# Performance work log

Hardware: AMD Instinct MI355X
Metric: run time of the kernel (lower is better)

The kernel has to match this reference:

```python
import jax, jax.numpy as jnp
import numpy as np

EPS = 1e-5

def _layernorm(x, g, b):
    mu = jnp.mean(x, axis=-1, keepdims=True)
    var = jnp.mean(jnp.square(x - mu), axis=-1, keepdims=True)
    return (x - mu) * jax.lax.rsqrt(var + EPS) * g + b

def _mlp(x, w1, b1, w2, b2):
    h = jax.nn.gelu(jnp.einsum('bnd,dh->bnh', x, w1) + b1, approximate=False)
    return jnp.einsum('bnh,hd->bnd', h, w2) + b2

def setup_inputs() -> dict:
    key = jax.random.key(0)
    B, N, D, H = 2, 8192, 1024, 4096
    ks = jax.random.split(key, 12)
    s1 = 1.0 / np.sqrt(D)
    s2 = 1.0 / np.sqrt(H)
    return {
        'x': jax.random.normal(ks[0], (B, N, D), dtype=jnp.float32),
        'mask': jax.random.randint(ks[1], (B, N), 0, 2) > 0,
        'g_rgb': jnp.ones((D,), jnp.float32),
        'b_rgb': jnp.zeros((D,), jnp.float32),
        'w1_rgb': jax.random.normal(ks[2], (D, H), dtype=jnp.float32) * s1,
        'b1_rgb': jnp.zeros((H,), jnp.float32),
        'w2_rgb': jax.random.normal(ks[3], (H, D), dtype=jnp.float32) * s2,
        'b2_rgb': jnp.zeros((D,), jnp.float32),
        'g_expr': jnp.ones((D,), jnp.float32),
        'b_expr': jnp.zeros((D,), jnp.float32),
        'w1_expr': jax.random.normal(ks[4], (D, H), dtype=jnp.float32) * s1,
        'b1_expr': jnp.zeros((H,), jnp.float32),
        'w2_expr': jax.random.normal(ks[5], (H, D), dtype=jnp.float32) * s2,
        'b2_expr': jnp.zeros((D,), jnp.float32),
    }

def reference(x, mask, g_rgb, b_rgb, w1_rgb, b1_rgb, w2_rgb, b2_rgb,
              g_expr, b_expr, w1_expr, b1_expr, w2_expr, b2_expr):
    # Per-token routing: rgb expert where mask, expr expert where ~mask.
    # LayerNorm+MLP are pointwise per token, so dense compute + select is
    # mathematically identical to the torch gather->compute->scatter.
    z_rgb = _mlp(_layernorm(x, g_rgb, b_rgb), w1_rgb, b1_rgb, w2_rgb, b2_rgb)
    z_expr = _mlp(_layernorm(x, g_expr, b_expr), w1_expr, b1_expr, w2_expr, b2_expr)
    z = jnp.where(mask[..., None], z_rgb, z_expr)
    return z.astype(jnp.float16)  # torch scatters into a float16 buffer
```

## Files before the change

### kernel.cpp

```cpp
#include <hip/hip_runtime.h>
#include <hip/hip_bf16.h>
#include <hip/hip_fp16.h>

#define D_ 1024
#define H_ 4096
#define NTOK 16384
#define MPAD 16512

typedef __attribute__((ext_vector_type(8))) short bf16x8;
typedef __attribute__((ext_vector_type(4))) float f32x4;

static __device__ __forceinline__ unsigned short f2bf(float f) {
  union { float f; unsigned u; } x; x.f = f;
  unsigned u = x.u + 0x7fffu + ((x.u >> 16) & 1u);
  return (unsigned short)(u >> 16);
}

static __device__ __forceinline__ void gld16(const void* g, void* l) {
  __builtin_amdgcn_global_load_lds(
      (const __attribute__((address_space(1))) unsigned int*)g,
      (__attribute__((address_space(3))) unsigned int*)l, 16, 0, 0);
}

static __device__ __forceinline__ float gelu_fast(float x) {
  const float z = x * (1.5957691216f + 0.0713548163f * x * x);
  return x * __builtin_amdgcn_rcpf(1.0f + __expf(-z));
}

__global__ __launch_bounds__(256) void transpose4_kernel(
    const float* __restrict__ w1r, const float* __restrict__ w1e,
    const float* __restrict__ w2r, const float* __restrict__ w2e,
    unsigned short* __restrict__ o1r, unsigned short* __restrict__ o1e,
    unsigned short* __restrict__ o2r, unsigned short* __restrict__ o2e) {
  __shared__ float tile[32][33];
  const int t = blockIdx.x;
  const float* src; unsigned short* dst; int R, C, tl;
  if (t < 4096)       { src = w1r; dst = o1r; R = D_; C = H_; tl = t; }
  else if (t < 8192)  { src = w1e; dst = o1e; R = D_; C = H_; tl = t - 4096; }
  else if (t < 12288) { src = w2r; dst = o2r; R = H_; C = D_; tl = t - 8192; }
  else                { src = w2e; dst = o2e; R = H_; C = D_; tl = t - 12288; }
  const int tc = C >> 5;
  const int r0 = (tl / tc) * 32, c0 = (tl % tc) * 32;
  const int tx = threadIdx.x & 31, ty = threadIdx.x >> 5;
#pragma unroll
  for (int i = 0; i < 32; i += 8)
    tile[ty + i][tx] = src[(size_t)(r0 + ty + i) * C + c0 + tx];
  __syncthreads();
#pragma unroll
  for (int i = 0; i < 32; i += 8)
    dst[(size_t)(c0 + ty + i) * R + r0 + tx] = f2bf(tile[tx][ty + i]);
}

__global__ __launch_bounds__(256) void compact_kernel(
    const int* __restrict__ mask, int* __restrict__ perm, int* __restrict__ counts) {
  const int NT = 256, CH = NTOK / NT;
  __shared__ int sm[NTOK];
  __shared__ int wsum[4];
  const int t = threadIdx.x;
  const int ln = t & 63, wv = t >> 6;
  for (int i = t; i < NTOK; i += NT) sm[i] = mask[i];
  for (int i = t; i < MPAD; i += NT) perm[i] = -1;
  __syncthreads();
  const int base = t * CH;
  int cnt = 0;
  for (int i = 0; i < CH; ++i) cnt += (sm[base + i] != 0);
  int sc = cnt;
#pragma unroll
  for (int o = 1; o < 64; o <<= 1) {
    int u = __shfl_up(sc, o, 64);
    if (ln >= o) sc += u;
  }
  if (ln == 63) wsum[wv] = sc;
  __syncthreads();
  int woff = 0;
#pragma unroll
  for (int j = 0; j < 4; ++j) woff += (j < wv) ? wsum[j] : 0;
  const int total1 = wsum[0] + wsum[1] + wsum[2] + wsum[3];
  if (t == 0) { counts[0] = total1; counts[1] = NTOK - total1; }
  const int excl = woff + sc - cnt;
  const int expr_base = ((total1 + 127) >> 7) << 7;
  int p1 = excl;
  int p0 = expr_base + (base - excl);
  for (int i = 0; i < CH; ++i) {
    const int idx = base + i;
    if (sm[idx] != 0) perm[p1++] = idx; else perm[p0++] = idx;
  }
}

__global__ __launch_bounds__(256) void ln_kernel(
    const float* __restrict__ x, const int* __restrict__ mask,
    const int* __restrict__ perm,
    const float* __restrict__ g_rgb, const float* __restrict__ b_rgb,
    const float* __restrict__ g_expr, const float* __restrict__ b_expr,
    unsigned short* __restrict__ xln) {
  const int i = blockIdx.x;
  const int t = perm[i];
  if (t < 0) return;
  const int tid = threadIdx.x;
  const float4 v = ((const float4*)(x + (size_t)t * D_))[tid];
  float s = v.x + v.y + v.z + v.w;
  float ss = v.x * v.x + v.y * v.y + v.z * v.z + v.w * v.w;
#pragma unroll
  for (int o = 32; o > 0; o >>= 1) {
    s += __shfl_xor(s, o, 64);
    ss += __shfl_xor(ss, o, 64);
  }
  __shared__ float red[8];
  const int wv = tid >> 6, ln = tid & 63;
  if (ln == 0) { red[wv] = s; red[4 + wv] = ss; }
  __syncthreads();
  s = red[0] + red[1] + red[2] + red[3];
  ss = red[4] + red[5] + red[6] + red[7];
  const float mu = s * (1.0f / D_);
  const float var = ss * (1.0f / D_) - mu * mu;
  const float rs = rsqrtf(var + 1e-5f);
  const bool rgb = mask[t] != 0;
  const float4 gv = ((const float4*)(rgb ? g_rgb : g_expr))[tid];
  const float4 bv = ((const float4*)(rgb ? b_rgb : b_expr))[tid];
  const unsigned short o0 = f2bf((v.x - mu) * rs * gv.x + bv.x);
  const unsigned short o1 = f2bf((v.y - mu) * rs * gv.y + bv.y);
  const unsigned short o2 = f2bf((v.z - mu) * rs * gv.z + bv.z);
  const unsigned short o3 = f2bf((v.w - mu) * rs * gv.w + bv.w);
  uint2 pk;
  pk.x = (unsigned)o0 | ((unsigned)o1 << 16);
  pk.y = (unsigned)o2 | ((unsigned)o3 << 16);
  *((uint2*)(xln + (size_t)i * D_ + tid * 4)) = pk;
}

template <int EP, int K, int N>
__global__ __launch_bounds__(256) void gemm_kernel(
    const unsigned short* __restrict__ A,
    const unsigned short* __restrict__ Wt_rgb,
    const unsigned short* __restrict__ Wt_expr,
    const float* __restrict__ bias_rgb,
    const float* __restrict__ bias_expr,
    const int* __restrict__ counts,
    const int* __restrict__ perm,
    void* __restrict__ OutP) {
  constexpr int BM = 128, BN = 128, BK = 64;
  constexpr int MT = MPAD / BM;
  constexpr int NT = N / BN;
  const int tid = threadIdx.x;
  const int id = blockIdx.x;
  const int xcd = id & 7;
  const int slot = id >> 3;
  const int p = xcd * ((MT * NT) / 8) + slot;
  const int m0 = (p / NT) * BM;
  const int n0 = (p % NT) * BN;
  const int cnt_rgb = counts[0];
  const unsigned short* Wt = (m0 < cnt_rgb) ? Wt_rgb : Wt_expr;
  const float* bias = (m0 < cnt_rgb) ? bias_rgb : bias_expr;

  __shared__ unsigned short As[BM * BK];
  __shared__ unsigned short Bs[BN * BK];

  f32x4 acc[4][4] = {};

  const int lane = tid & 63, wave = tid >> 6;
  const int wm = (wave & 1) * 64, wn = (wave >> 1) * 64;
  const int quad = lane >> 4, l16 = lane & 15;

  const char* Abase = (const char*)A;
  const char* Wbase = (const char*)Wt;
  const char* AsB = (const char*)As;
  const char* BsB = (const char*)Bs;

  int ag[4], bg[4], sl[4];
#pragma unroll
  for (int it = 0; it < 4; ++it) {
    const int s = it * 256 + tid;
    const int row = s >> 3;
    const int ks = ((s ^ row) & 7) * 8;
    ag[it] = ((m0 + row) * K + ks) * 2;
    bg[it] = ((n0 + row) * K + ks) * 2;
    sl[it] = s * 16;
  }
  int aoff[2][4], boff[2][4];
#pragma unroll
  for (int hh = 0; hh < 2; ++hh) {
    const int cb = hh * 4 + quad;
#pragma unroll
    for (int mi = 0; mi < 4; ++mi) {
      const int row = wm + mi * 16 + l16;
      aoff[hh][mi] = (row * BK + (((cb ^ row) & 7) << 3)) * 2;
    }
#pragma unroll
    for (int ni = 0; ni < 4; ++ni) {
      const int row = wn + ni * 16 + l16;
      boff[hh][ni] = (row * BK + (((cb ^ row) & 7) << 3)) * 2;
    }
  }

  for (int k0 = 0; k0 < K; k0 += BK) {
#pragma unroll
    for (int it = 0; it < 4; ++it) {
      gld16(Abase + ag[it], (void*)(AsB + sl[it]));
      gld16(Wbase + bg[it], (void*)(BsB + sl[it]));
      ag[it] += BK * 2;
      bg[it] += BK * 2;
    }
    __syncthreads();
#pragma unroll
    for (int hh = 0; hh < 2; ++hh) {
      bf16x8 a[4], b[4];
#pragma unroll
      for (int mi = 0; mi < 4; ++mi) a[mi] = *(const bf16x8*)(AsB + aoff[hh][mi]);
#pragma unroll
      for (int ni = 0; ni < 4; ++ni) b[ni] = *(const bf16x8*)(BsB + boff[hh][ni]);
#pragma unroll
      for (int mi = 0; mi < 4; ++mi)
#pragma unroll
        for (int ni = 0; ni < 4; ++ni)
          acc[mi][ni] = __builtin_amdgcn_mfma_f32_16x16x32_bf16(a[mi], b[ni], acc[mi][ni], 0, 0, 0);
    }
    __syncthreads();
  }

  float bv[4];
#pragma unroll
  for (int ni = 0; ni < 4; ++ni) bv[ni] = bias[n0 + wn + ni * 16 + l16];

#pragma unroll
  for (int mi = 0; mi < 4; ++mi) {
#pragma unroll
    for (int r = 0; r < 4; ++r) {
      const int row = m0 + wm + mi * 16 + quad * 4 + r;
      if (EP == 0) {
        unsigned short* orow = (unsigned short*)OutP + (size_t)row * N + n0 + wn + l16;
#pragma unroll
        for (int ni = 0; ni < 4; ++ni) {
          orow[ni * 16] = f2bf(gelu_fast(acc[mi][ni][r] + bv[ni]));
        }
      } else {
        const int p2 = perm[row];
        if (p2 < 0) continue;
        float* orow = (float*)OutP + (size_t)p2 * N + n0 + wn + l16;
#pragma unroll
        for (int ni = 0; ni < 4; ++ni) {
          float v = acc[mi][ni][r] + bv[ni];
          orow[ni * 16] = __half2float(__float2half_rn(v));
        }
      }
    }
  }
}

extern "C" void kernel_launch(void* const* d_in, const int* in_sizes, int n_in,
                              void* d_out, int out_size, void* d_ws, size_t ws_size,
                              hipStream_t stream) {
  const float* x       = (const float*)d_in[0];
  const int*   mask    = (const int*)d_in[1];
  const float* g_rgb   = (const float*)d_in[2];
  const float* b_rgb   = (const float*)d_in[3];
  const float* w1_rgb  = (const float*)d_in[4];
  const float* b1_rgb  = (const float*)d_in[5];
  const float* w2_rgb  = (const float*)d_in[6];
  const float* b2_rgb  = (const float*)d_in[7];
  const float* g_expr  = (const float*)d_in[8];
  const float* b_expr  = (const float*)d_in[9];
  const float* w1_expr = (const float*)d_in[10];
  const float* b1_expr = (const float*)d_in[11];
  const float* w2_expr = (const float*)d_in[12];
  const float* b2_expr = (const float*)d_in[13];

  char* w = (char*)d_ws;
  int* counts               = (int*)(w + 0);
  int* perm                 = (int*)(w + 256);
  unsigned short* w1t_rgb   = (unsigned short*)(w + 66560);
  unsigned short* w1t_expr  = (unsigned short*)(w + 8455168);
  unsigned short* w2t_rgb   = (unsigned short*)(w + 16843776);
  unsigned short* w2t_expr  = (unsigned short*)(w + 25232384);
  unsigned short* xln       = (unsigned short*)(w + 33620992);
  unsigned short* h         = (unsigned short*)(w + 67437568);

  compact_kernel<<<1, 256, 0, stream>>>(mask, perm, counts);

  transpose4_kernel<<<16384, 256, 0, stream>>>(
      w1_rgb, w1_expr, w2_rgb, w2_expr, w1t_rgb, w1t_expr, w2t_rgb, w2t_expr);

  ln_kernel<<<MPAD, 256, 0, stream>>>(x, mask, perm, g_rgb, b_rgb, g_expr, b_expr, xln);

  gemm_kernel<0, D_, H_><<<dim3((H_ / 128) * (MPAD / 128)), 256, 0, stream>>>(
      xln, w1t_rgb, w1t_expr, b1_rgb, b1_expr, counts, perm, h);

  gemm_kernel<1, H_, D_><<<dim3((D_ / 128) * (MPAD / 128)), 256, 0, stream>>>(
      h, w2t_rgb, w2t_expr, b2_rgb, b2_expr, counts, perm, d_out);
}
```

Before: 592.0 us.

## Add 256x256-tile 8-wave pipelined GEMM for first MLP layer

Replaces the first GEMM (LN output × W1 with GELU epilogue) with a new kernel using 256x256 output tiles, 512 threads, double-buffered LDS filled by direct global-to-LDS loads, and interleaved barrier-scheduled MFMA phases with raised priority. Expert segments are now padded to 256 rows so each tile uses a single expert weight, which grows MPAD and shifts the workspace offsets. The larger tile raises arithmetic intensity and cuts redundant global traffic. In exchange it adds a little padding compute and heavy register and LDS use: 128 KB of shared memory per block and 128 accumulator floats per thread.

```diff
diff --git a/kernel.cpp b/kernel.cpp
--- a/kernel.cpp
+++ b/kernel.cpp
@@ -5,7 +5,7 @@
 #define D_ 1024
 #define H_ 4096
 #define NTOK 16384
-#define MPAD 16512
+#define MPAD 16640
 
 typedef __attribute__((ext_vector_type(8))) short bf16x8;
 typedef __attribute__((ext_vector_type(4))) float f32x4;
@@ -78,7 +78,7 @@
   const int total1 = wsum[0] + wsum[1] + wsum[2] + wsum[3];
   if (t == 0) { counts[0] = total1; counts[1] = NTOK - total1; }
   const int excl = woff + sc - cnt;
-  const int expr_base = ((total1 + 127) >> 7) << 7;
+  const int expr_base = ((total1 + 255) >> 8) << 8;
   int p1 = excl;
   int p0 = expr_base + (base - excl);
   for (int i = 0; i < CH; ++i) {
@@ -125,6 +125,183 @@
   pk.x = (unsigned)o0 | ((unsigned)o1 << 16);
   pk.y = (unsigned)o2 | ((unsigned)o3 << 16);
   *((uint2*)(xln + (size_t)i * D_ + tid * 4)) = pk;
+}
+
+template <int K, int N>
+__global__ __launch_bounds__(512, 2) void gemm8_kernel(
+    const unsigned short* __restrict__ A,
+    const unsigned short* __restrict__ Wt_rgb,
+    const unsigned short* __restrict__ Wt_expr,
+    const float* __restrict__ bias_rgb,
+    const float* __restrict__ bias_expr,
+    const int* __restrict__ counts,
+    unsigned short* __restrict__ Out) {
+  constexpr int MT = MPAD / 256;
+  constexpr int NT = N / 256;
+  constexpr int ntk = K / 64;
+  constexpr int KH2 = 128 * K * 2;
+
+  const int tid = threadIdx.x;
+  const int id = blockIdx.x;
+  const int xcd = id & 7;
+  const int slot = id >> 3;
+  const int p = xcd * ((MT * NT) / 8) + slot;
+  const int m0 = (p / NT) * 256;
+  const int n0 = (p % NT) * 256;
+  const int cnt_rgb = counts[0];
+  const unsigned short* Wt = (m0 < cnt_rgb) ? Wt_rgb : Wt_expr;
+  const float* bias = (m0 < cnt_rgb) ? bias_rgb : bias_expr;
+
+  __shared__ unsigned short As[2][256 * 64];
+  __shared__ unsigned short Bs[2][256 * 64];
+
+  const int lane = tid & 63, wave = tid >> 6;
+  const int wr = wave >> 2, wc = wave & 3;
+  const int quad = lane >> 4, l16 = lane & 15;
+
+  f32x4 acc[8][4] = {};
+
+  const char* Abase = (const char*)A;
+  const char* Wbase = (const char*)Wt;
+
+  int agK0, agK1, bgK0, bgK1, sl0, sl1;
+  {
+    const int s0 = tid, s1 = 512 + tid;
+    const int r0 = s0 >> 3, r1 = s1 >> 3;
+    const int ks0 = ((s0 ^ r0) & 7) * 8, ks1 = ((s1 ^ r1) & 7) * 8;
+    agK0 = ((m0 + r0) * K + ks0) * 2;  agK1 = ((m0 + r1) * K + ks1) * 2;
+    bgK0 = ((n0 + r0) * K + ks0) * 2;  bgK1 = ((n0 + r1) * K + ks1) * 2;
+    sl0 = s0 * 16;  sl1 = s1 * 16;
+  }
+
+  int aoffL[2][2][4];
+  int boffL[2][4];
+#pragma unroll
+  for (int kk = 0; kk < 2; ++kk) {
+    const int cb = kk * 4 + quad;
+#pragma unroll
+    for (int mh = 0; mh < 2; ++mh)
+#pragma unroll
+      for (int mi = 0; mi < 4; ++mi) {
+        const int row = wr * 128 + mh * 64 + mi * 16 + l16;
+        aoffL[kk][mh][mi] = (row * 64 + ((cb ^ row) & 7) * 8) * 2;
+      }
+#pragma unroll
+    for (int ni = 0; ni < 4; ++ni) {
+      const int row = wc * 64 + ni * 16 + l16;
+      boffL[kk][ni] = (row * 64 + ((cb ^ row) & 7) * 8) * 2;
+    }
+  }
+
+  bf16x8 a0, a1, a2, a3;
+  bf16x8 bb[4];
+
+#define STAGE_A(T1, HA, Q) do { \
+    gld16(Abase + agK0 + (HA) * KH2 + (T1) * 128, (char*)As + (Q) * 32768 + (HA) * 16384 + sl0); \
+    gld16(Abase + agK1 + (HA) * KH2 + (T1) * 128, (char*)As + (Q) * 32768 + (HA) * 16384 + sl1); \
+  } while (0)
+#define STAGE_B(T2, HB, Q) do { \
+    gld16(Wbase + bgK0 + (HB) * KH2 + (T2) * 128, (char*)Bs + (Q) * 32768 + (HB) * 16384 + sl0); \
+    gld16(Wbase + bgK1 + (HB) * KH2 + (T2) * 128, (char*)Bs + (Q) * 32768 + (HB) * 16384 + sl1); \
+  } while (0)
+#define RD_A(P_, KK, MH) do { \
+    const char* _ab = (const char*)As + (P_) * 32768; \
+    a0 = *(const bf16x8*)(_ab + aoffL[KK][MH][0]); \
+    a1 = *(const bf16x8*)(_ab + aoffL[KK][MH][1]); \
+    a2 = *(const bf16x8*)(_ab + aoffL[KK][MH][2]); \
+    a3 = *(const bf16x8*)(_ab + aoffL[KK][MH][3]); \
+  } while (0)
+#define RD_B(P_, KK) do { \
+    const char* _bp = (const char*)Bs + (P_) * 32768; \
+    bb[0] = *(const bf16x8*)(_bp + boffL[KK][0]); \
+    bb[1] = *(const bf16x8*)(_bp + boffL[KK][1]); \
+    bb[2] = *(const bf16x8*)(_bp + boffL[KK][2]); \
+    bb[3] = *(const bf16x8*)(_bp + boffL[KK][3]); \
+  } while (0)
+#define MFMA16(MO) do { \
+    acc[(MO)+0][0] = __builtin_amdgcn_mfma_f32_16x16x32_bf16(a0, bb[0], acc[(MO)+0][0], 0, 0, 0); \
+    acc[(MO)+0][1] = __builtin_amdgcn_mfma_f32_16x16x32_bf16(a0, bb[1], acc[(MO)+0][1], 0, 0, 0); \
+    acc[(MO)+0][2] = __builtin_amdgcn_mfma_f32_16x16x32_bf16(a0, bb[2], acc[(MO)+0][2], 0, 0, 0); \
+    acc[(MO)+0][3] = __builtin_amdgcn_mfma_f32_16x16x32_bf16(a0, bb[3], acc[(MO)+0][3], 0, 0, 0); \
+    acc[(MO)+1][0] = __builtin_amdgcn_mfma_f32_16x16x32_bf16(a1, bb[0], acc[(MO)+1][0], 0, 0, 0); \
+    acc[(MO)+1][1] = __builtin_amdgcn_mfma_f32_16x16x32_bf16(a1, bb[1], acc[(MO)+1][1], 0, 0, 0); \
+    acc[(MO)+1][2] = __builtin_amdgcn_mfma_f32_16x16x32_bf16(a1, bb[2], acc[(MO)+1][2], 0, 0, 0); \
+    acc[(MO)+1][3] = __builtin_amdgcn_mfma_f32_16x16x32_bf16(a1, bb[3], acc[(MO)+1][3], 0, 0, 0); \
+    acc[(MO)+2][0] = __builtin_amdgcn_mfma_f32_16x16x32_bf16(a2, bb[0], acc[(MO)+2][0], 0, 0, 0); \
+    acc[(MO)+2][1] = __builtin_amdgcn_mfma_f32_16x16x32_bf16(a2, bb[1], acc[(MO)+2][1], 0, 0, 0); \
+    acc[(MO)+2][2] = __builtin_amdgcn_mfma_f32_16x16x32_bf16(a2, bb[2], acc[(MO)+2][2], 0, 0, 0); \
+    acc[(MO)+2][3] = __builtin_amdgcn_mfma_f32_16x16x32_bf16(a2, bb[3], acc[(MO)+2][3], 0, 0, 0); \
+    acc[(MO)+3][0] = __builtin_amdgcn_mfma_f32_16x16x32_bf16(a3, bb[0], acc[(MO)+3][0], 0, 0, 0); \
+    acc[(MO)+3][1] = __builtin_amdgcn_mfma_f32_16x16x32_bf16(a3, bb[1], acc[(MO)+3][1], 0, 0, 0); \
+    acc[(MO)+3][2] = __builtin_amdgcn_mfma_f32_16x16x32_bf16(a3, bb[2], acc[(MO)+3][2], 0, 0, 0); \
+    acc[(MO)+3][3] = __builtin_amdgcn_mfma_f32_16x16x32_bf16(a3, bb[3], acc[(MO)+3][3], 0, 0, 0); \
+  } while (0)
+
+#define KTILE(T_, P_, SA_, SB_, VMC_) do { \
+     \
+    RD_B(P_, 0); RD_A(P_, 0, 0); \
+    if (SA_) STAGE_A((T_) + 1, 0, (P_) ^ 1); \
+    __builtin_amdgcn_s_barrier(); \
+    __builtin_amdgcn_s_setprio(1); MFMA16(0); __builtin_amdgcn_s_setprio(0); \
+    __builtin_amdgcn_s_barrier(); \
+     \
+    RD_A(P_, 0, 1); \
+    if (SA_) STAGE_A((T_) + 1, 1, (P_) ^ 1); \
+    __builtin_amdgcn_s_barrier(); \
+    __builtin_amdgcn_s_setprio(1); MFMA16(4); __builtin_amdgcn_s_setprio(0); \
+    __builtin_amdgcn_s_barrier(); \
+     \
+    RD_B(P_, 1); RD_A(P_, 1, 0); \
+    __builtin_amdgcn_s_barrier(); \
+    __builtin_amdgcn_s_setprio(1); MFMA16(0); __builtin_amdgcn_s_setprio(0); \
+    __builtin_amdgcn_s_barrier(); \
+     \
+    RD_A(P_, 1, 1); \
+    if (SB_) { STAGE_B((T_) + 2, 0, P_); STAGE_B((T_) + 2, 1, P_); } \
+    __builtin_amdgcn_s_barrier(); \
+    __builtin_amdgcn_s_setprio(1); MFMA16(4); __builtin_amdgcn_s_setprio(0); \
+    if ((VMC_) == 4) { asm volatile("s_waitcnt vmcnt(4)" ::: "memory"); } \
+    else if ((VMC_) == 0) { asm volatile("s_waitcnt vmcnt(0)" ::: "memory"); } \
+    __builtin_amdgcn_sched_barrier(0); \
+    __builtin_amdgcn_s_barrier(); \
+  } while (0)
+
+  STAGE_A(0, 0, 0); STAGE_A(0, 1, 0);
+  STAGE_B(0, 0, 0); STAGE_B(0, 1, 0);
+  STAGE_B(1, 0, 1); STAGE_B(1, 1, 1);
+  asm volatile("s_waitcnt vmcnt(4)" ::: "memory");
+  __builtin_amdgcn_sched_barrier(0);
+  __builtin_amdgcn_s_barrier();
+
+  for (int tt = 0; tt < ntk / 2 - 1; ++tt) {
+    const int t0 = tt * 2;
+    KTILE(t0, 0, 1, 1, 4);
+    KTILE(t0 + 1, 1, 1, 1, 4);
+  }
+  KTILE(ntk - 2, 0, 1, 0, 0);
+  KTILE(ntk - 1, 1, 0, 0, -1);
+
+#undef KTILE
+#undef MFMA16
+#undef RD_B
+#undef RD_A
+#undef STAGE_B
+#undef STAGE_A
+
+  float bv[4];
+#pragma unroll
+  for (int ni = 0; ni < 4; ++ni) bv[ni] = bias[n0 + wc * 64 + ni * 16 + l16];
+#pragma unroll
+  for (int mi = 0; mi < 8; ++mi) {
+#pragma unroll
+    for (int r = 0; r < 4; ++r) {
+      const int row = m0 + wr * 128 + mi * 16 + quad * 4 + r;
+      unsigned short* orow = Out + (size_t)row * N + n0 + wc * 64 + l16;
+#pragma unroll
+      for (int ni = 0; ni < 4; ++ni)
+        orow[ni * 16] = f2bf(gelu_fast(acc[mi][ni][r] + bv[ni]));
+    }
+  }
 }
 
 template <int EP, int K, int N>
@@ -266,12 +443,12 @@
   char* w = (char*)d_ws;
   int* counts               = (int*)(w + 0);
   int* perm                 = (int*)(w + 256);
-  unsigned short* w1t_rgb   = (unsigned short*)(w + 66560);
-  unsigned short* w1t_expr  = (unsigned short*)(w + 8455168);
-  unsigned short* w2t_rgb   = (unsigned short*)(w + 16843776);
-  unsigned short* w2t_expr  = (unsigned short*)(w + 25232384);
-  unsigned short* xln       = (unsigned short*)(w + 33620992);
-  unsigned short* h         = (unsigned short*)(w + 67437568);
+  unsigned short* w1t_rgb   = (unsigned short*)(w + 66816);
+  unsigned short* w1t_expr  = (unsigned short*)(w + 8455424);
+  unsigned short* w2t_rgb   = (unsigned short*)(w + 16844032);
+  unsigned short* w2t_expr  = (unsigned short*)(w + 25232640);
+  unsigned short* xln       = (unsigned short*)(w + 33621248);
+  unsigned short* h         = (unsigned short*)(w + 67699968);
 
   compact_kernel<<<1, 256, 0, stream>>>(mask, perm, counts);
 
@@ -280,8 +457,8 @@
 
   ln_kernel<<<MPAD, 256, 0, stream>>>(x, mask, perm, g_rgb, b_rgb, g_expr, b_expr, xln);
 
-  gemm_kernel<0, D_, H_><<<dim3((H_ / 128) * (MPAD / 128)), 256, 0, stream>>>(
-      xln, w1t_rgb, w1t_expr, b1_rgb, b1_expr, counts, perm, h);
+  gemm8_kernel<D_, H_><<<dim3((MPAD / 256) * (H_ / 256)), 512, 0, stream>>>(
+      xln, w1t_rgb, w1t_expr, b1_rgb, b1_expr, counts, h);
 
   gemm_kernel<1, H_, D_><<<dim3((D_ / 128) * (MPAD / 128)), 256, 0, stream>>>(
       h, w2t_rgb, w2t_expr, b2_rgb, b2_expr, counts, perm, d_out);
```

New measurement: 574.6 us. 1.03x faster.
